# Kernel tuning notes

Measured on AMD Instinct MI355X. Metric: run time of the kernel, lower is better.

## Reference

```python
import jax, jax.numpy as jnp
from jax import lax
import numpy as np

NUM_CLASSES = 85742  # MS1M-scale classifier
C = 512              # feature channels
KH = KW = 1          # 1x1 conv classifier kernel
B = 512              # batch size
H = W = 7            # feature map spatial size


def setup_inputs() -> dict:
    key = jax.random.key(0)
    kx, kw = jax.random.split(key)
    x = jax.random.normal(kx, (B, C, H, W), dtype=jnp.float32)
    # labels: all distinct so torch's labels.unique() has deterministic size B
    labels = jnp.arange(B, dtype=jnp.int64)
    weight = jax.random.normal(kw, (NUM_CLASSES, C, KH, KW), dtype=jnp.float32) * 0.02
    bias = jnp.zeros((NUM_CLASSES,), dtype=jnp.float32)  # requires_grad=False in torch
    return {"x": x, "labels": labels, "weight": weight, "bias": bias}


def reference(x, labels, weight, bias):
    # Partial-FC style: gather the unique-label subset of the classifier weight,
    # then run a conv producing logits only over that subset.
    # jnp.unique with static size=B is jit-compatible; labels are all distinct here.
    labels_unique = jnp.unique(labels, size=labels.shape[0], fill_value=0)  # [U], sorted
    w_sub = weight[labels_unique]   # [U, C, KH, KW] irregular gather
    b_sub = bias[labels_unique]     # [U]
    logits = lax.conv_general_dilated(
        x, w_sub,
        window_strides=(1, 1), padding="VALID",
        dimension_numbers=("NCHW", "OIHW", "NCHW"),
    )  # [B, U, H, W]
    return logits + b_sub[None, :, None, None]
```

## Files before the change

### kernel.cpp

```cpp
#include <hip/hip_runtime.h>
#include <hip/hip_bf16.h>

#define NUM_CLASSES 85742
#define CIN   512
#define BATCH 512
#define HW    49
#define NPAD  64
#define UDIM  512
#define KT    16
#define NSTEP (CIN / KT)

typedef short bf16x8 __attribute__((ext_vector_type(8)));
typedef float f32x16 __attribute__((ext_vector_type(16)));
typedef __hip_bfloat16 bf16;

__device__ __forceinline__ void gload_lds16(const void* g, void* l) {
  __builtin_amdgcn_global_load_lds(
      (const __attribute__((address_space(1))) void*)g,
      (__attribute__((address_space(3))) void*)l, 16, 0, 0);
}

__device__ __forceinline__ void split_bf16(float v, bf16& h, bf16& l) {
  h = __float2bfloat16(v);
  l = __float2bfloat16(v - __bfloat162float(h));
}

__device__ __forceinline__ f32x16 zero16() {
  f32x16 r;
#pragma unroll
  for (int i = 0; i < 16; ++i) r[i] = 0.f;
  return r;
}

#define MFMA32(A, B, C) __builtin_amdgcn_mfma_f32_32x32x16_bf16((A), (B), (C), 0, 0, 0)

__global__ void sort_gather(const int* __restrict__ labels,
                            const float* __restrict__ bias,
                            int* __restrict__ sorted,
                            float* __restrict__ bsub)
{
  __shared__ int sl[BATCH];
  const int i = threadIdx.x;
  const int stride = (labels[1] == 0) ? 2 : 1;
  const int li = labels[i * stride];
  sl[i] = li;
  __syncthreads();
  int rank = 0;
#pragma unroll 8
  for (int j = 0; j < BATCH; ++j) rank += (sl[j] < li) ? 1 : 0;
  sorted[rank] = li;
  bsub[rank]   = bias[li];
}

__global__ void wprep(const float* __restrict__ weight,
                      const int* __restrict__ sorted,
                      bf16* __restrict__ whi, bf16* __restrict__ wlo)
{
  const int u   = blockIdx.x;
  const int lbl = sorted[u];
  const float* wrow = weight + (size_t)lbl * CIN;
  for (int k = threadIdx.x; k < CIN; k += 256) {
    float v = wrow[k];
    bf16 h, l;
    split_bf16(v, h, l);
    const int s = k >> 4, kq = (k >> 3) & 1, j = k & 7;
    const size_t idx = (((size_t)(s * 2 + kq)) * UDIM + u) * 8 + j;
    whi[idx] = h;
    wlo[idx] = l;
  }
}

__global__ __launch_bounds__(512, 4) void convcls_main(
    const float* __restrict__ x,
    const bf16* __restrict__ whi, const bf16* __restrict__ wlo,
    const float* __restrict__ bsub,
    float* __restrict__ out)
{
  __shared__ __attribute__((aligned(16))) bf16 WhB[2][2][UDIM][8];
  __shared__ __attribute__((aligned(16))) bf16 WlB[2][2][UDIM][8];
  __shared__ __attribute__((aligned(16))) bf16 XhB[2][2][NPAD][8];
  __shared__ __attribute__((aligned(16))) bf16 XlB[2][2][NPAD][8];

  const int b    = blockIdx.x;
  const int tid  = threadIdx.x;
  const int wave = tid >> 6;
  const int lane = tid & 63;
  const int l31  = lane & 31;
  const int lq   = lane >> 5;

  f32x16 acc00 = zero16(), acc01 = zero16(), acc10 = zero16(), acc11 = zero16();

  const float* xb = x + (size_t)b * CIN * HW;
  const int kk = tid >> 5;
  const int hs = tid & 31;
  const int kq = kk >> 3, kj = kk & 7;

  {
    float x0 = xb[(size_t)kk * HW + hs];
    float x1 = (hs + 32 < HW) ? xb[(size_t)kk * HW + hs + 32] : 0.f;
    bf16 h, l;
    split_bf16(x0, h, l); XhB[0][kq][hs][kj] = h;      XlB[0][kq][hs][kj] = l;
    split_bf16(x1, h, l); XhB[0][kq][hs + 32][kj] = h; XlB[0][kq][hs + 32][kj] = l;
#pragma unroll
    for (int i = 0; i < 2; ++i) {
      const int c = wave * 2 + i;
      gload_lds16(whi + (size_t)c * 512 + lane * 8, (char*)&WhB[0][0][0][0] + c * 1024);
      gload_lds16(wlo + (size_t)c * 512 + lane * 8, (char*)&WlB[0][0][0][0] + c * 1024);
    }
  }
  __syncthreads();

  const int u0 = wave * 64 + l31;
  for (int s = 0; s < NSTEP; ++s) {
    const int cur = s & 1, nxt = cur ^ 1;
    const bool pf = (s + 1 < NSTEP);
    float x0 = 0.f, x1 = 0.f;
    if (pf) {
      const float* xs = xb + (size_t)(s + 1) * KT * HW;
      x0 = xs[(size_t)kk * HW + hs];
      x1 = (hs + 32 < HW) ? xs[(size_t)kk * HW + hs + 32] : 0.f;
      const size_t wbase = (size_t)(s + 1) * (2 * UDIM * 8);
#pragma unroll
      for (int i = 0; i < 2; ++i) {
        const int c = wave * 2 + i;
        gload_lds16(whi + wbase + (size_t)c * 512 + lane * 8,
                    (char*)&WhB[nxt][0][0][0] + c * 1024);
        gload_lds16(wlo + wbase + (size_t)c * 512 + lane * 8,
                    (char*)&WlB[nxt][0][0][0] + c * 1024);
      }
    }

    bf16x8 bh0 = *(const bf16x8*)&XhB[cur][lq][l31][0];
    bf16x8 bl0 = *(const bf16x8*)&XlB[cur][lq][l31][0];
    bf16x8 bh1 = *(const bf16x8*)&XhB[cur][lq][32 + l31][0];
    bf16x8 bl1 = *(const bf16x8*)&XlB[cur][lq][32 + l31][0];
    bf16x8 ah0 = *(const bf16x8*)&WhB[cur][lq][u0][0];
    bf16x8 al0 = *(const bf16x8*)&WlB[cur][lq][u0][0];
    bf16x8 ah1 = *(const bf16x8*)&WhB[cur][lq][u0 + 32][0];
    bf16x8 al1 = *(const bf16x8*)&WlB[cur][lq][u0 + 32][0];

    acc00 = MFMA32(ah0, bh0, acc00);
    acc01 = MFMA32(ah0, bh1, acc01);
    acc10 = MFMA32(ah1, bh0, acc10);
    acc11 = MFMA32(ah1, bh1, acc11);
    acc00 = MFMA32(ah0, bl0, acc00);
    acc01 = MFMA32(ah0, bl1, acc01);
    acc10 = MFMA32(ah1, bl0, acc10);
    acc11 = MFMA32(ah1, bl1, acc11);
    acc00 = MFMA32(al0, bh0, acc00);
    acc01 = MFMA32(al0, bh1, acc01);
    acc10 = MFMA32(al1, bh0, acc10);
    acc11 = MFMA32(al1, bh1, acc11);

    if (pf) {
      bf16 h, l;
      split_bf16(x0, h, l); XhB[nxt][kq][hs][kj] = h;      XlB[nxt][kq][hs][kj] = l;
      split_bf16(x1, h, l); XhB[nxt][kq][hs + 32][kj] = h; XlB[nxt][kq][hs + 32][kj] = l;
    }
    __syncthreads();
  }

  const int ub = wave * 64;
#pragma unroll
  for (int r = 0; r < 16; ++r) {
    const int urow = (r & 3) + 8 * (r >> 2) + 4 * lq;
    {
      const int u = ub + urow;
      const float bs = bsub[u];
      out[((size_t)b * UDIM + u) * HW + l31] = acc00[r] + bs;
      if (l31 + 32 < HW) out[((size_t)b * UDIM + u) * HW + 32 + l31] = acc01[r] + bs;
    }
    {
      const int u = ub + 32 + urow;
      const float bs = bsub[u];
      out[((size_t)b * UDIM + u) * HW + l31] = acc10[r] + bs;
      if (l31 + 32 < HW) out[((size_t)b * UDIM + u) * HW + 32 + l31] = acc11[r] + bs;
    }
  }
}

extern "C" void kernel_launch(void* const* d_in, const int* in_sizes, int n_in,
                              void* d_out, int out_size, void* d_ws, size_t ws_size,
                              hipStream_t stream)
{
  const float* x      = (const float*)d_in[0];
  const int*   labels = (const int*)d_in[1];
  const float* weight = (const float*)d_in[2];
  const float* bias   = (const float*)d_in[3];
  float*       out    = (float*)d_out;

  int*   sorted = (int*)d_ws;
  float* bsub   = (float*)((char*)d_ws + 2048);
  bf16*  whi    = (bf16*)((char*)d_ws + 4096);
  bf16*  wlo    = (bf16*)((char*)d_ws + 4096 + 512 * 1024);

  sort_gather<<<1, BATCH, 0, stream>>>(labels, bias, sorted, bsub);
  wprep<<<UDIM, 256, 0, stream>>>(weight, sorted, whi, wlo);
  convcls_main<<<BATCH, 512, 0, stream>>>(x, whi, wlo, bsub, out);
}
```

Baseline: 306.1 us.

## Retile conv GEMM over flattened batch-spatial dim with 128x256 blocks

Flattens batch and spatial positions into one M dimension of 25088 and tiles it in 128-row blocks, with each block covering half of the 512 classes. This removes the padding of 49 positions up to 64 per image that wasted MFMA work, and block order is swizzled for L2 reuse of the weight halves. The bf16 hi/lo split is rewritten as explicit bit arithmetic, and x loads become 4-wide per thread. The cost is more blocks, each reloading weights and x, and scattered output addresses because tiles cross image boundaries.

```diff
diff --git a/kernel.cpp b/kernel.cpp
--- a/kernel.cpp
+++ b/kernel.cpp
@@ -1,18 +1,23 @@
 #include <hip/hip_runtime.h>
 #include <hip/hip_bf16.h>
 
-#define NUM_CLASSES 85742
-#define CIN   512
-#define BATCH 512
-#define HW    49
-#define NPAD  64
-#define UDIM  512
-#define KT    16
-#define NSTEP (CIN / KT)
-
-typedef short bf16x8 __attribute__((ext_vector_type(8)));
-typedef float f32x16 __attribute__((ext_vector_type(16)));
-typedef __hip_bfloat16 bf16;
+#define CIN    512
+#define BATCH  512
+#define HW     49
+#define UDIM   512
+#define MTOT   (BATCH * HW)
+#define MT     128
+#define NMB    (MTOT / MT)
+#define UHALF  256
+#define KT     16
+#define NSTEP  (CIN / KT)
+#define NBLK   (NMB * 2)
+
+typedef short  bf16x8 __attribute__((ext_vector_type(8)));
+typedef short  s16x4  __attribute__((ext_vector_type(4)));
+typedef float  f32x16 __attribute__((ext_vector_type(16)));
+
+#define MFMA32(A, B, C) __builtin_amdgcn_mfma_f32_32x32x16_bf16((A), (B), (C), 0, 0, 0)
 
 __device__ __forceinline__ void gload_lds16(const void* g, void* l) {
   __builtin_amdgcn_global_load_lds(
@@ -20,9 +25,13 @@
       (__attribute__((address_space(3))) void*)l, 16, 0, 0);
 }
 
-__device__ __forceinline__ void split_bf16(float v, bf16& h, bf16& l) {
-  h = __float2bfloat16(v);
-  l = __float2bfloat16(v - __bfloat162float(h));
+__device__ __forceinline__ void split2(float v, unsigned short& h, unsigned short& l) {
+  unsigned int b  = __float_as_uint(v);
+  unsigned int hb = (b + 0x7FFFu + ((b >> 16) & 1u)) >> 16;
+  float hf        = __uint_as_float(hb << 16);
+  unsigned int lb = __float_as_uint(v - hf);
+  h = (unsigned short)hb;
+  l = (unsigned short)((lb + 0x7FFFu + ((lb >> 16) & 1u)) >> 16);
 }
 
 __device__ __forceinline__ f32x16 zero16() {
@@ -31,8 +40,6 @@
   for (int i = 0; i < 16; ++i) r[i] = 0.f;
   return r;
 }
-
-#define MFMA32(A, B, C) __builtin_amdgcn_mfma_f32_32x32x16_bf16((A), (B), (C), 0, 0, 0)
 
 __global__ void sort_gather(const int* __restrict__ labels,
                             const float* __restrict__ bias,
@@ -54,15 +61,15 @@
 
 __global__ void wprep(const float* __restrict__ weight,
                       const int* __restrict__ sorted,
-                      bf16* __restrict__ whi, bf16* __restrict__ wlo)
+                      unsigned short* __restrict__ whi,
+                      unsigned short* __restrict__ wlo)
 {
   const int u   = blockIdx.x;
   const int lbl = sorted[u];
   const float* wrow = weight + (size_t)lbl * CIN;
   for (int k = threadIdx.x; k < CIN; k += 256) {
-    float v = wrow[k];
-    bf16 h, l;
-    split_bf16(v, h, l);
+    unsigned short h, l;
+    split2(wrow[k], h, l);
     const int s = k >> 4, kq = (k >> 3) & 1, j = k & 7;
     const size_t idx = (((size_t)(s * 2 + kq)) * UDIM + u) * 8 + j;
     whi[idx] = h;
@@ -72,109 +79,122 @@
 
 __global__ __launch_bounds__(512, 4) void convcls_main(
     const float* __restrict__ x,
-    const bf16* __restrict__ whi, const bf16* __restrict__ wlo,
+    const unsigned short* __restrict__ whi,
+    const unsigned short* __restrict__ wlo,
     const float* __restrict__ bsub,
     float* __restrict__ out)
 {
-  __shared__ __attribute__((aligned(16))) bf16 WhB[2][2][UDIM][8];
-  __shared__ __attribute__((aligned(16))) bf16 WlB[2][2][UDIM][8];
-  __shared__ __attribute__((aligned(16))) bf16 XhB[2][2][NPAD][8];
-  __shared__ __attribute__((aligned(16))) bf16 XlB[2][2][NPAD][8];
-
-  const int b    = blockIdx.x;
+  __shared__ __attribute__((aligned(16))) unsigned short WhB[2][2][UHALF][8];
+  __shared__ __attribute__((aligned(16))) unsigned short WlB[2][2][UHALF][8];
+  __shared__ __attribute__((aligned(16))) unsigned short XhB[2][2][MT][8];
+  __shared__ __attribute__((aligned(16))) unsigned short XlB[2][2][MT][8];
+
+  const int bid = blockIdx.x;
+  const int swz = (bid & 7) * (NBLK / 8) + (bid >> 3);
+  const int uh  = swz / NMB;
+  const int mb  = swz - uh * NMB;
+
   const int tid  = threadIdx.x;
-  const int wave = tid >> 6;
-  const int lane = tid & 63;
-  const int l31  = lane & 31;
-  const int lq   = lane >> 5;
-
-  f32x16 acc00 = zero16(), acc01 = zero16(), acc10 = zero16(), acc11 = zero16();
-
-  const float* xb = x + (size_t)b * CIN * HW;
-  const int kk = tid >> 5;
-  const int hs = tid & 31;
-  const int kq = kk >> 3, kj = kk & 7;
+  const int wave = tid >> 6, lane = tid & 63;
+  const int l31  = lane & 31, lq = lane >> 5;
+
+  const int mloc = tid & 127;
+  const int ks   = tid >> 7;
+  const int kqs  = ks >> 1;
+  const int j0   = (ks & 1) * 4;
+  const int mg   = mb * MT + mloc;
+  const int bimg = mg / HW;
+  const int hwp  = mg - bimg * HW;
+  const float* xsrc = x + (size_t)bimg * (CIN * HW) + hwp;
+
+  const size_t wsrcbase =
+      ((size_t)(wave >> 2) * UDIM + uh * UHALF + (wave & 3) * 64) * 8 + lane * 8;
+
+  f32x16 a00 = zero16(), a01 = zero16(), a10 = zero16(), a11 = zero16();
+
+  const int uoff = (wave & 3) * 64;
+  const int moff = (wave >> 2) * 64;
 
   {
-    float x0 = xb[(size_t)kk * HW + hs];
-    float x1 = (hs + 32 < HW) ? xb[(size_t)kk * HW + hs + 32] : 0.f;
-    bf16 h, l;
-    split_bf16(x0, h, l); XhB[0][kq][hs][kj] = h;      XlB[0][kq][hs][kj] = l;
-    split_bf16(x1, h, l); XhB[0][kq][hs + 32][kj] = h; XlB[0][kq][hs + 32][kj] = l;
-#pragma unroll
-    for (int i = 0; i < 2; ++i) {
-      const int c = wave * 2 + i;
-      gload_lds16(whi + (size_t)c * 512 + lane * 8, (char*)&WhB[0][0][0][0] + c * 1024);
-      gload_lds16(wlo + (size_t)c * 512 + lane * 8, (char*)&WlB[0][0][0][0] + c * 1024);
-    }
+    float v[4];
+#pragma unroll
+    for (int i = 0; i < 4; ++i) v[i] = xsrc[(size_t)(ks * 4 + i) * HW];
+    gload_lds16(whi + wsrcbase, (char*)&WhB[0][0][0][0] + wave * 1024);
+    gload_lds16(wlo + wsrcbase, (char*)&WlB[0][0][0][0] + wave * 1024);
+    s16x4 ph, pl;
+#pragma unroll
+    for (int i = 0; i < 4; ++i) {
+      unsigned short h, l; split2(v[i], h, l);
+      ph[i] = (short)h; pl[i] = (short)l;
+    }
+    *(s16x4*)&XhB[0][kqs][mloc][j0] = ph;
+    *(s16x4*)&XlB[0][kqs][mloc][j0] = pl;
   }
   __syncthreads();
 
-  const int u0 = wave * 64 + l31;
   for (int s = 0; s < NSTEP; ++s) {
     const int cur = s & 1, nxt = cur ^ 1;
     const bool pf = (s + 1 < NSTEP);
-    float x0 = 0.f, x1 = 0.f;
+    float v[4];
     if (pf) {
-      const float* xs = xb + (size_t)(s + 1) * KT * HW;
-      x0 = xs[(size_t)kk * HW + hs];
-      x1 = (hs + 32 < HW) ? xs[(size_t)kk * HW + hs + 32] : 0.f;
-      const size_t wbase = (size_t)(s + 1) * (2 * UDIM * 8);
-#pragma unroll
-      for (int i = 0; i < 2; ++i) {
-        const int c = wave * 2 + i;
-        gload_lds16(whi + wbase + (size_t)c * 512 + lane * 8,
-                    (char*)&WhB[nxt][0][0][0] + c * 1024);
-        gload_lds16(wlo + wbase + (size_t)c * 512 + lane * 8,
-                    (char*)&WlB[nxt][0][0][0] + c * 1024);
+      const size_t so = (size_t)(s + 1) * (2 * UDIM * 8);
+      gload_lds16(whi + so + wsrcbase, (char*)&WhB[nxt][0][0][0] + wave * 1024);
+      gload_lds16(wlo + so + wsrcbase, (char*)&WlB[nxt][0][0][0] + wave * 1024);
+#pragma unroll
+      for (int i = 0; i < 4; ++i)
+        v[i] = xsrc[(size_t)((s + 1) * KT + ks * 4 + i) * HW];
+    }
+
+    bf16x8 ah0 = *(const bf16x8*)&WhB[cur][lq][uoff + l31][0];
+    bf16x8 ah1 = *(const bf16x8*)&WhB[cur][lq][uoff + 32 + l31][0];
+    bf16x8 al0 = *(const bf16x8*)&WlB[cur][lq][uoff + l31][0];
+    bf16x8 al1 = *(const bf16x8*)&WlB[cur][lq][uoff + 32 + l31][0];
+    bf16x8 bh0 = *(const bf16x8*)&XhB[cur][lq][moff + l31][0];
+    bf16x8 bh1 = *(const bf16x8*)&XhB[cur][lq][moff + 32 + l31][0];
+    bf16x8 bl0 = *(const bf16x8*)&XlB[cur][lq][moff + l31][0];
+    bf16x8 bl1 = *(const bf16x8*)&XlB[cur][lq][moff + 32 + l31][0];
+
+    a00 = MFMA32(ah0, bh0, a00);  a01 = MFMA32(ah0, bh1, a01);
+    a10 = MFMA32(ah1, bh0, a10);  a11 = MFMA32(ah1, bh1, a11);
+    a00 = MFMA32(ah0, bl0, a00);  a01 = MFMA32(ah0, bl1, a01);
+    a10 = MFMA32(ah1, bl0, a10);  a11 = MFMA32(ah1, bl1, a11);
+    a00 = MFMA32(al0, bh0, a00);  a01 = MFMA32(al0, bh1, a01);
+    a10 = MFMA32(al1, bh0, a10);  a11 = MFMA32(al1, bh1, a11);
+
+    if (pf) {
+      s16x4 ph, pl;
+#pragma unroll
+      for (int i = 0; i < 4; ++i) {
+        unsigned short h, l; split2(v[i], h, l);
+        ph[i] = (short)h; pl[i] = (short)l;
       }
-    }
-
-    bf16x8 bh0 = *(const bf16x8*)&XhB[cur][lq][l31][0];
-    bf16x8 bl0 = *(const bf16x8*)&XlB[cur][lq][l31][0];
-    bf16x8 bh1 = *(const bf16x8*)&XhB[cur][lq][32 + l31][0];
-    bf16x8 bl1 = *(const bf16x8*)&XlB[cur][lq][32 + l31][0];
-    bf16x8 ah0 = *(const bf16x8*)&WhB[cur][lq][u0][0];
-    bf16x8 al0 = *(const bf16x8*)&WlB[cur][lq][u0][0];
-    bf16x8 ah1 = *(const bf16x8*)&WhB[cur][lq][u0 + 32][0];
-    bf16x8 al1 = *(const bf16x8*)&WlB[cur][lq][u0 + 32][0];
-
-    acc00 = MFMA32(ah0, bh0, acc00);
-    acc01 = MFMA32(ah0, bh1, acc01);
-    acc10 = MFMA32(ah1, bh0, acc10);
-    acc11 = MFMA32(ah1, bh1, acc11);
-    acc00 = MFMA32(ah0, bl0, acc00);
-    acc01 = MFMA32(ah0, bl1, acc01);
-    acc10 = MFMA32(ah1, bl0, acc10);
-    acc11 = MFMA32(ah1, bl1, acc11);
-    acc00 = MFMA32(al0, bh0, acc00);
-    acc01 = MFMA32(al0, bh1, acc01);
-    acc10 = MFMA32(al1, bh0, acc10);
-    acc11 = MFMA32(al1, bh1, acc11);
-
-    if (pf) {
-      bf16 h, l;
-      split_bf16(x0, h, l); XhB[nxt][kq][hs][kj] = h;      XlB[nxt][kq][hs][kj] = l;
-      split_bf16(x1, h, l); XhB[nxt][kq][hs + 32][kj] = h; XlB[nxt][kq][hs + 32][kj] = l;
+      *(s16x4*)&XhB[nxt][kqs][mloc][j0] = ph;
+      *(s16x4*)&XlB[nxt][kqs][mloc][j0] = pl;
     }
     __syncthreads();
   }
 
-  const int ub = wave * 64;
+  const int u0g = uh * UHALF + uoff;
+  const int m0g = mb * MT + moff;
+  const int mA  = m0g + l31,      mB = m0g + 32 + l31;
+  const int bA  = mA / HW,        hA = mA - bA * HW;
+  const int bB  = mB / HW,        hB = mB - bB * HW;
+  float* oA = out + (size_t)bA * (UDIM * HW) + hA;
+  float* oB = out + (size_t)bB * (UDIM * HW) + hB;
 #pragma unroll
   for (int r = 0; r < 16; ++r) {
     const int urow = (r & 3) + 8 * (r >> 2) + 4 * lq;
     {
-      const int u = ub + urow;
+      const int u = u0g + urow;
       const float bs = bsub[u];
-      out[((size_t)b * UDIM + u) * HW + l31] = acc00[r] + bs;
-      if (l31 + 32 < HW) out[((size_t)b * UDIM + u) * HW + 32 + l31] = acc01[r] + bs;
+      oA[(size_t)u * HW] = a00[r] + bs;
+      oB[(size_t)u * HW] = a01[r] + bs;
     }
     {
-      const int u = ub + 32 + urow;
+      const int u = u0g + 32 + urow;
       const float bs = bsub[u];
-      out[((size_t)b * UDIM + u) * HW + l31] = acc10[r] + bs;
-      if (l31 + 32 < HW) out[((size_t)b * UDIM + u) * HW + 32 + l31] = acc11[r] + bs;
+      oA[(size_t)u * HW] = a10[r] + bs;
+      oB[(size_t)u * HW] = a11[r] + bs;
     }
   }
 }
@@ -189,12 +209,12 @@
   const float* bias   = (const float*)d_in[3];
   float*       out    = (float*)d_out;
 
-  int*   sorted = (int*)d_ws;
-  float* bsub   = (float*)((char*)d_ws + 2048);
-  bf16*  whi    = (bf16*)((char*)d_ws + 4096);
-  bf16*  wlo    = (bf16*)((char*)d_ws + 4096 + 512 * 1024);
+  int*            sorted = (int*)d_ws;
+  float*          bsub   = (float*)((char*)d_ws + 2048);
+  unsigned short* whi    = (unsigned short*)((char*)d_ws + 4096);
+  unsigned short* wlo    = (unsigned short*)((char*)d_ws + 4096 + 512 * 1024);
 
   sort_gather<<<1, BATCH, 0, stream>>>(labels, bias, sorted, bsub);
   wprep<<<UDIM, 256, 0, stream>>>(weight, sorted, whi, wlo);
-  convcls_main<<<BATCH, 512, 0, stream>>>(x, whi, wlo, bsub, out);
-}
+  convcls_main<<<NBLK, 512, 0, stream>>>(x, whi, wlo, bsub, out);
+}
```

After: 314.0 us. 2.6% more time.
